# Performance work log

Hardware: AMD Instinct MI355X
Metric: run time of the kernel (lower is better)

## Reference

```python
import jax, jax.numpy as jnp
import numpy as np

N_NODES = 30000
N_EDGES = 300000
C = 16          # multiplicity of input scalars and of each output irrep
SH_SPLITS = [(0, 1), (1, 4), (4, 9)]  # l=0,1,2 slices of edge_sh


def setup_inputs() -> dict:
    key = jax.random.key(0)
    ks = jax.random.split(key, 7)
    node_feat = jax.random.normal(ks[0], (N_NODES, C), dtype=jnp.float32)
    edge_index = jax.random.randint(ks[1], (2, N_EDGES), 0, N_NODES, dtype=jnp.int64)
    edge_sh = jax.random.normal(ks[2], (N_EDGES, 9), dtype=jnp.float32)
    edge_radial = jax.random.uniform(ks[3], (N_EDGES, 16), dtype=jnp.float32)
    W1 = jax.random.normal(ks[4], (16, 64), dtype=jnp.float32)     # radial net layer 1
    W2 = jax.random.normal(ks[5], (64, 3 * C * C), dtype=jnp.float32)  # -> tp.weight_numel = 768
    W_si = jax.random.normal(ks[6], (C, C), dtype=jnp.float32)     # self-interaction 0e->0e
    return {"node_feat": node_feat, "edge_index": edge_index, "edge_sh": edge_sh,
            "edge_radial": edge_radial, "W1": W1, "W2": W2, "W_si": W_si}


def reference(node_feat, edge_index, edge_sh, edge_radial, W1, W2, W_si):
    N, c = node_feat.shape  # c == C
    src, dst = edge_index[0], edge_index[1]

    # Radial MLP (e3nn FullyConnectedNet style: weight / sqrt(fan_in), silu, no bias)
    h = jax.nn.silu(edge_radial @ (W1 / jnp.sqrt(jnp.asarray(W1.shape[0], W1.dtype))))
    tpw = h @ (W2 / jnp.sqrt(jnp.asarray(W2.shape[0], W2.dtype)))  # (E, 768)
    tpw = tpw.reshape(-1, 3, c, c)  # (E, l, u, v)

    # Gather source scalars and mix multiplicities per path (0e x l -> l, CG = identity)
    x = node_feat[src]                                   # (E, C)
    mix = jnp.einsum('eu,eluv->elv', x, tpw) / jnp.sqrt(jnp.asarray(c, x.dtype))  # (E,3,C)

    # Outer product with each SH degree; e3nn mul-major layout (v, m)
    msgs = []
    for l, (a, b) in enumerate(SH_SPLITS):
        m = mix[:, l, :, None] * edge_sh[:, None, a:b]   # (E, C, 2l+1)
        msgs.append(m.reshape(m.shape[0], -1))
    messages = jnp.concatenate(msgs, axis=-1)            # (E, 144)

    # Scatter-add to destination nodes
    agg = jax.ops.segment_sum(messages, dst, num_segments=N)  # (N, 144)

    # Self-interaction: equivariant Linear, only 0e->0e path; l>0 outputs are zero
    si_scalar = node_feat @ (W_si / jnp.sqrt(jnp.asarray(c, node_feat.dtype)))  # (N, C)
    si = jnp.concatenate([si_scalar, jnp.zeros((N, 8 * c), si_scalar.dtype)], axis=-1)
    return agg + si
```

## Files before the change

### kernel.cpp

```cpp
#include <hip/hip_runtime.h>


typedef _Float16 f16x2 __attribute__((ext_vector_type(2)));
typedef _Float16 f16x8 __attribute__((ext_vector_type(8)));
typedef __fp16  g16x2 __attribute__((ext_vector_type(2)));
typedef float f32x4 __attribute__((ext_vector_type(4)));

union AFrag { unsigned int u[4]; f16x2 h2[4]; f16x8 v; };
union BFrag { uint4 u4; f16x8 v; };
union HW { g16x2 g; f16x2 f; unsigned int u; };


__global__ __launch_bounds__(256)
void prep_kernel(const float* __restrict__ W2, const float* __restrict__ W1,
                 _Float16* __restrict__ bfrag, _Float16* __restrict__ w1frag,
                 const int* __restrict__ ei, int* __restrict__ counts, int E) {
    int t = blockIdx.x * 256 + threadIdx.x;
    if (t < E) atomicAdd(&counts[ei[E + t] + 1], 1);
    if (t < 96 * 512) {
        int f = t >> 9;
        int rr = t & 511;
        int lane = rr >> 3, j = rr & 7;
        int ks = f / 3, nt = f - 3 * ks;
        int q = lane >> 4, c = lane & 15;
        int ku = ks * 32 + q * 8 + j;
        int k = ku >> 4, u = ku & 15;
        int n = nt * 16 + c;
        int l = n >> 4, v = n & 15;
        float val = W2[(size_t)k * 768 + l * 256 + u * 16 + v] * 0.03125f;
        bfrag[t] = (_Float16)val;
    }
    if (t < 2048) {
        int nt = t >> 9, rr = t & 511;
        int lane = rr >> 3, j = rr & 7;
        int q = lane >> 4, c = lane & 15;
        int u = q * 8 + j;
        float val = (q < 2) ? W1[u * 64 + nt * 16 + c] * 0.25f : 0.0f;
        w1frag[t] = (_Float16)val;
    }
}

__global__ __launch_bounds__(1024)
void scan_kernel(int* __restrict__ data, int n_pad) {
    __shared__ int wsum[16];
    __shared__ int carry_s;
    int tid = threadIdx.x, lane = tid & 63, wid = tid >> 6;
    if (tid == 0) carry_s = 0;
    __syncthreads();
    for (int base = 0; base < n_pad; base += 32768) {
        int beg = base + tid * 32;
        int4 c0[8];
        #pragma unroll
        for (int j = 0; j < 8; ++j)
            c0[j] = *(const int4*)(data + beg + j * 4);
        int s = 0;
        #pragma unroll
        for (int j = 0; j < 8; ++j) s += c0[j].x + c0[j].y + c0[j].z + c0[j].w;

        int v = s;
        #pragma unroll
        for (int off = 1; off < 64; off <<= 1) {
            int t = __shfl_up(v, off, 64);
            if (lane >= off) v += t;
        }
        if (lane == 63) wsum[wid] = v;
        __syncthreads();
        if (wid == 0 && lane < 16) {
            int w = wsum[lane];
            #pragma unroll
            for (int off = 1; off < 16; off <<= 1) {
                int t = __shfl_up(w, off, 16);
                if (lane >= off) w += t;
            }
            wsum[lane] = w;
        }
        __syncthreads();
        int run = carry_s + (v - s) + (wid > 0 ? wsum[wid - 1] : 0);
        #pragma unroll
        for (int j = 0; j < 8; ++j) {
            int4 o;
            run += c0[j].x; o.x = run;
            run += c0[j].y; o.y = run;
            run += c0[j].z; o.z = run;
            run += c0[j].w; o.w = run;
            *(int4*)(data + beg + j * 4) = o;
        }
        __syncthreads();
        if (tid == 1023) carry_s = run;
        __syncthreads();
    }
}


__global__ __launch_bounds__(64, 4)
void edge_mfma_kernel(const float* __restrict__ nf, const int* __restrict__ ei,
                      const float* __restrict__ radial,
                      const _Float16* __restrict__ w1frag,
                      const float* __restrict__ sh,
                      const _Float16* __restrict__ bfrag,
                      const int* __restrict__ offs, int* __restrict__ curs,
                      _Float16* __restrict__ mixs, _Float16* __restrict__ shs, int E) {
    __shared__ unsigned int h_lds[64][32];

    int lane = threadIdx.x & 63;
    int r_ = lane & 15;
    int q  = lane >> 4;
    int qh = q >> 1;
    int ul = (q & 1) * 8;
    unsigned int sel = qh ? 0x03020302u : 0x01000100u;

    int ebase = blockIdx.x * 64;

    HW xp[4][4];
    #pragma unroll
    for (int m = 0; m < 4; ++m) {
        int e = ebase + m * 16 + r_; if (e >= E) e = E - 1;
        int src = ei[e];
        const float* xpp = nf + (size_t)src * 16 + ul;
        float4 a = *(const float4*)xpp;
        float4 b = *(const float4*)(xpp + 4);
        xp[m][0].g = __builtin_amdgcn_cvt_pkrtz(a.x, a.y);
        xp[m][1].g = __builtin_amdgcn_cvt_pkrtz(a.z, a.w);
        xp[m][2].g = __builtin_amdgcn_cvt_pkrtz(b.x, b.y);
        xp[m][3].g = __builtin_amdgcn_cvt_pkrtz(b.z, b.w);
    }

    int p = 0;
    {
        int e = ebase + lane;
        if (e < E) {
            int dst = ei[E + e];
            p = offs[dst] + atomicAdd(&curs[dst], 1);
            const float* s = sh + (size_t)e * 9;
            float4 s03 = *(const float4*)s;
            float4 s47 = *(const float4*)(s + 4);
            float s8 = s[8];
            unsigned int* d = (unsigned int*)(shs + (size_t)p * 10);
            HW w0, w1, w2, w3, w4;
            w0.g = __builtin_amdgcn_cvt_pkrtz(s03.x, s03.y);
            w1.g = __builtin_amdgcn_cvt_pkrtz(s03.z, s03.w);
            w2.g = __builtin_amdgcn_cvt_pkrtz(s47.x, s47.y);
            w3.g = __builtin_amdgcn_cvt_pkrtz(s47.z, s47.w);
            w4.g = __builtin_amdgcn_cvt_pkrtz(s8, 0.0f);
            d[0] = w0.u; d[1] = w1.u; d[2] = w2.u; d[3] = w3.u; d[4] = w4.u;
        }
    }

    {
        BFrag wf[4];
        #pragma unroll
        for (int nt = 0; nt < 4; ++nt)
            wf[nt].u4 = *(const uint4*)(w1frag + (size_t)nt * 512 + lane * 8);

        #pragma unroll
        for (int m = 0; m < 4; ++m) {
            AFrag ra;
            if (q < 2) {
                int e = ebase + m * 16 + r_; if (e >= E) e = E - 1;
                const float* rp = radial + (size_t)e * 16 + q * 8;
                float4 a = *(const float4*)rp;
                float4 b = *(const float4*)(rp + 4);
                HW t0, t1, t2, t3;
                t0.g = __builtin_amdgcn_cvt_pkrtz(a.x, a.y);
                t1.g = __builtin_amdgcn_cvt_pkrtz(a.z, a.w);
                t2.g = __builtin_amdgcn_cvt_pkrtz(b.x, b.y);
                t3.g = __builtin_amdgcn_cvt_pkrtz(b.z, b.w);
                ra.u[0] = t0.u; ra.u[1] = t1.u; ra.u[2] = t2.u; ra.u[3] = t3.u;
            } else {
                ra.u[0] = 0; ra.u[1] = 0; ra.u[2] = 0; ra.u[3] = 0;
            }
            #pragma unroll
            for (int nt = 0; nt < 4; ++nt) {
                f32x4 z4 = __builtin_amdgcn_mfma_f32_16x16x32_f16(
                    ra.v, wf[nt].v, (f32x4){0.f, 0.f, 0.f, 0.f}, 0, 0, 0);
                #pragma unroll
                for (int i = 0; i < 4; ++i) {
                    float z = z4[i];
                    float h = z * __builtin_amdgcn_rcpf(1.0f + __expf(-z));
                    float hn = __shfl_xor(h, 1);
                    if (!(r_ & 1)) {
                        int el = m * 16 + q * 4 + i;
                        HW w; w.g = __builtin_amdgcn_cvt_pkrtz(h, hn);
                        h_lds[el][((nt << 3) + (r_ >> 1)) ^ (el & 31)] = w.u;
                    }
                }
            }
        }
    }

    f32x4 acc[4][3];
    #pragma unroll
    for (int m = 0; m < 4; ++m)
        #pragma unroll
        for (int nt = 0; nt < 3; ++nt)
            acc[m][nt] = (f32x4){0.f, 0.f, 0.f, 0.f};

    #pragma unroll 2
    for (int ks = 0; ks < 32; ++ks) {
        BFrag b[3];
        #pragma unroll
        for (int nt = 0; nt < 3; ++nt)
            b[nt].u4 = *(const uint4*)(bfrag + (size_t)(ks * 3 + nt) * 512 + lane * 8);
        #pragma unroll
        for (int m = 0; m < 4; ++m) {
            int el = m * 16 + r_;
            unsigned int hw = h_lds[el][ks ^ (el & 31)];
            HW hv; hv.u = __builtin_amdgcn_perm(hw, hw, sel);
            AFrag a;
            #pragma unroll
            for (int p2 = 0; p2 < 4; ++p2)
                a.h2[p2] = hv.f * xp[m][p2].f;
            #pragma unroll
            for (int nt = 0; nt < 3; ++nt)
                acc[m][nt] = __builtin_amdgcn_mfma_f32_16x16x32_f16(a.v, b[nt].v, acc[m][nt], 0, 0, 0);
        }
    }

    unsigned int* mixu = (unsigned int*)mixs;
    #pragma unroll
    for (int m = 0; m < 4; ++m) {
        #pragma unroll
        for (int i = 0; i < 4; ++i) {
            int el = m * 16 + q * 4 + i;
            int e = ebase + el;
            int pe = __shfl(p, el, 64);
            if (e < E) {
                HW pr; pr.g = __builtin_amdgcn_cvt_pkrtz(acc[m][0][i], acc[m][1][i]);
                mixu[(size_t)pe * 24 + r_] = pr.u;
                mixs[(size_t)pe * 48 + 32 + r_] = (_Float16)acc[m][2][i];
            }
        }
    }
}


__global__ __launch_bounds__(256)
void gather_kernel(const _Float16* __restrict__ mixs, const _Float16* __restrict__ shs,
                   const int* __restrict__ offs,
                   const float* __restrict__ nf, const float* __restrict__ Wsi,
                   float* __restrict__ out, int N) {
    int node = blockIdx.x * 4 + (threadIdx.x >> 6);
    if (node >= N) return;
    int lane = threadIdx.x & 63;

    auto chmap = [](int c, int& hi, int& si) {
        if (c < 16)      { hi = 2 * c;           si = 0; }
        else if (c < 64) { int t = c - 16; hi = 2 * (t / 3) + 1; si = 1 + t % 3; }
        else             { int t = c - 64; hi = 32 + t / 5;      si = 4 + t % 5; }
    };
    int hi0, si0, hi1, si1, hi2 = 0, si2 = 0;
    chmap(lane, hi0, si0);
    chmap(lane + 64, hi1, si1);
    if (lane < 16) chmap(lane + 128, hi2, si2);

    float g0[8], g1[8], g2[8];
    #pragma unroll
    for (int j = 0; j < 8; ++j) { g0[j] = 0.f; g1[j] = 0.f; g2[j] = 0.f; }

    int off = offs[node], end = offs[node + 1];
    int i = off;
    for (; i + 7 < end; i += 8) {
        #pragma unroll
        for (int j = 0; j < 8; ++j) {
            const _Float16* m = mixs + (size_t)(i + j) * 48;
            const _Float16* s = shs + (size_t)(i + j) * 10;
            g0[j] = fmaf((float)m[hi0], (float)s[si0], g0[j]);
            g1[j] = fmaf((float)m[hi1], (float)s[si1], g1[j]);
            if (lane < 16) g2[j] = fmaf((float)m[hi2], (float)s[si2], g2[j]);
        }
    }
    for (int j = 0; i < end; ++i, ++j) {
        const _Float16* m = mixs + (size_t)i * 48;
        const _Float16* s = shs + (size_t)i * 10;
        g0[j] = fmaf((float)m[hi0], (float)s[si0], g0[j]);
        g1[j] = fmaf((float)m[hi1], (float)s[si1], g1[j]);
        if (lane < 16) g2[j] = fmaf((float)m[hi2], (float)s[si2], g2[j]);
    }
    float a0 = (g0[0] + g0[1]) + (g0[2] + g0[3]) + ((g0[4] + g0[5]) + (g0[6] + g0[7]));
    float a1 = (g1[0] + g1[1]) + (g1[2] + g1[3]) + ((g1[4] + g1[5]) + (g1[6] + g1[7]));
    float a2 = (g2[0] + g2[1]) + (g2[2] + g2[3]) + ((g2[4] + g2[5]) + (g2[6] + g2[7]));

    if (lane < 16) {
        const float* xr = nf + (size_t)node * 16;
        float si = 0.0f;
        #pragma unroll
        for (int u = 0; u < 16; ++u)
            si = fmaf(xr[u], Wsi[u * 16 + lane], si);
        a0 = fmaf(si, 0.25f, a0);
    }

    float* orow = out + (size_t)node * 144;
    orow[lane] = a0;
    orow[lane + 64] = a1;
    if (lane < 16) orow[lane + 128] = a2;
}


__global__ __launch_bounds__(256)
void si_init_kernel(const float* __restrict__ nf, const float* __restrict__ Wsi,
                    float* __restrict__ out, int N) {
    int t = blockIdx.x * blockDim.x + threadIdx.x;
    int total = N * 144;
    if (t >= total) return;
    int n = t / 144;
    int c = t - n * 144;
    float val = 0.0f;
    if (c < 16) {
        const float* xr = nf + n * 16;
        #pragma unroll
        for (int u = 0; u < 16; ++u)
            val = fmaf(xr[u], Wsi[u * 16 + c], val);
        val *= 0.25f;
    }
    out[t] = val;
}

__global__ __launch_bounds__(256)
void edge_kernel_atomic(const float* __restrict__ nf, const int* __restrict__ ei,
                        const float* __restrict__ sh, const float* __restrict__ radial,
                        const float* __restrict__ W1, const float* __restrict__ W2,
                        float* __restrict__ out, int E) {
    int e = blockIdx.x * blockDim.x + threadIdx.x;
    if (e >= E) return;
    int src = ei[e];
    int dst = ei[E + e];
    float r[16], x[16];
    #pragma unroll
    for (int u = 0; u < 16; ++u) r[u] = radial[e * 16 + u] * 0.25f;
    #pragma unroll
    for (int u = 0; u < 16; ++u) x[u] = nf[src * 16 + u] * 0.03125f;
    float acc[48];
    #pragma unroll
    for (int j = 0; j < 48; ++j) acc[j] = 0.0f;
    for (int k = 0; k < 64; ++k) {
        float z = 0.0f;
        #pragma unroll
        for (int u = 0; u < 16; ++u) z = fmaf(r[u], W1[u * 64 + k], z);
        float hk = z / (1.0f + __expf(-z));
        const float* w2k = W2 + k * 768;
        #pragma unroll 4
        for (int u = 0; u < 16; ++u) {
            float p = hk * x[u];
            const float* w = w2k + u * 16;
            #pragma unroll
            for (int l = 0; l < 3; ++l)
                #pragma unroll
                for (int v = 0; v < 16; ++v)
                    acc[l * 16 + v] = fmaf(p, w[l * 256 + v], acc[l * 16 + v]);
        }
    }
    const float* she = sh + e * 9;
    float* orow = out + (long)dst * 144;
    #pragma unroll
    for (int v = 0; v < 16; ++v) atomicAdd(&orow[v], acc[v] * she[0]);
    #pragma unroll
    for (int v = 0; v < 16; ++v)
        for (int m = 0; m < 3; ++m)
            atomicAdd(&orow[16 + v * 3 + m], acc[16 + v] * she[1 + m]);
    #pragma unroll
    for (int v = 0; v < 16; ++v)
        for (int m = 0; m < 5; ++m)
            atomicAdd(&orow[64 + v * 5 + m], acc[32 + v] * she[4 + m]);
}


extern "C" void kernel_launch(void* const* d_in, const int* in_sizes, int n_in,
                              void* d_out, int out_size, void* d_ws, size_t ws_size,
                              hipStream_t stream) {
    const float* nf     = (const float*)d_in[0];
    const int*   ei     = (const int*)  d_in[1];
    const float* sh     = (const float*)d_in[2];
    const float* radial = (const float*)d_in[3];
    const float* W1     = (const float*)d_in[4];
    const float* W2     = (const float*)d_in[5];
    const float* Wsi    = (const float*)d_in[6];
    float* out = (float*)d_out;

    const int N = in_sizes[0] / 16;
    const int E = in_sizes[1] / 2;

    int n_scan = N + 1;
    int n_pad  = (n_scan + 32767) & ~32767;

    size_t mix_bytes  = (size_t)E * 48 * sizeof(_Float16);
    size_t offs_bytes = (size_t)n_pad * sizeof(int);
    size_t curs_bytes = (size_t)N * sizeof(int);
    size_t shs_bytes  = (size_t)E * 10 * sizeof(_Float16);
    size_t bfrag_off  = (mix_bytes + offs_bytes + curs_bytes + shs_bytes + 127) & ~(size_t)127;
    size_t bfrag_bytes = 96 * 512 * sizeof(_Float16);
    size_t w1f_off    = bfrag_off + bfrag_bytes;
    size_t w1f_bytes  = 2048 * sizeof(_Float16);
    size_t need = w1f_off + w1f_bytes;

    if (ws_size < need) {
        int total = N * 144;
        hipLaunchKernelGGL(si_init_kernel, dim3((total + 255) / 256), dim3(256), 0, stream,
                           nf, Wsi, out, N);
        hipLaunchKernelGGL(edge_kernel_atomic, dim3((E + 255) / 256), dim3(256), 0, stream,
                           nf, ei, sh, radial, W1, W2, out, E);
        return;
    }

    char* wsb = (char*)d_ws;
    _Float16* mixs = (_Float16*)wsb;
    int*   offs = (int*)(wsb + mix_bytes);
    int*   curs = (int*)(wsb + mix_bytes + offs_bytes);
    _Float16* shs = (_Float16*)(wsb + mix_bytes + offs_bytes + curs_bytes);
    _Float16* bfrag = (_Float16*)(wsb + bfrag_off);
    _Float16* w1frag = (_Float16*)(wsb + w1f_off);

    (void)hipMemsetAsync(offs, 0, offs_bytes + curs_bytes, stream);

    int eb256 = (E + 255) / 256;
    hipLaunchKernelGGL(prep_kernel, dim3(eb256), dim3(256), 0, stream,
                       W2, W1, bfrag, w1frag, ei, offs, E);
    hipLaunchKernelGGL(scan_kernel, dim3(1), dim3(1024), 0, stream, offs, n_pad);
    int eb64 = (E + 63) / 64;
    hipLaunchKernelGGL(edge_mfma_kernel, dim3(eb64), dim3(64), 0, stream,
                       nf, ei, radial, w1frag, sh, bfrag, offs, curs, mixs, shs, E);
    hipLaunchKernelGGL(gather_kernel, dim3((N + 3) / 4), dim3(256), 0, stream,
                       mixs, shs, offs, nf, Wsi, out, N);
}
```

Baseline: 132.7 us.

## Accumulate gather messages in packed fp16 with two edges per wavefront

Rewrites the per-node gather so each lane loads packed 32-bit half2 words of mix and SH values, and the wave splits into two 24-lane halves that each process alternate edges. Accumulation runs in packed fp16 and the halves are combined with shuffles at the end. The aim is fewer load instructions and fewer scalar conversions and FMAs per edge. The cost is precision: sums over many edges accumulated in fp16 may lose accuracy or overflow, and the output stores become strided and less coalesced.

```diff
diff --git a/kernel.cpp b/kernel.cpp
--- a/kernel.cpp
+++ b/kernel.cpp
@@ -242,57 +242,95 @@
     int node = blockIdx.x * 4 + (threadIdx.x >> 6);
     if (node >= N) return;
     int lane = threadIdx.x & 63;
-
-    auto chmap = [](int c, int& hi, int& si) {
-        if (c < 16)      { hi = 2 * c;           si = 0; }
-        else if (c < 64) { int t = c - 16; hi = 2 * (t / 3) + 1; si = 1 + t % 3; }
-        else             { int t = c - 64; hi = 32 + t / 5;      si = 4 + t % 5; }
-    };
-    int hi0, si0, hi1, si1, hi2 = 0, si2 = 0;
-    chmap(lane, hi0, si0);
-    chmap(lane + 64, hi1, si1);
-    if (lane < 16) chmap(lane + 128, hi2, si2);
-
-    float g0[8], g1[8], g2[8];
-    #pragma unroll
-    for (int j = 0; j < 8; ++j) { g0[j] = 0.f; g1[j] = 0.f; g2[j] = 0.f; }
+    int half = (lane >= 24 && lane < 48) ? 1 : 0;
+    int w = lane - half * 24;
+    bool active = lane < 48;
+    bool isP = active && (w < 16);
+    bool isQ = active && (w >= 16) && (w < 24);
+    int t = w - 16;
+
+    const unsigned int* mixw = (const unsigned int*)mixs;
+    const unsigned int* shw  = (const unsigned int*)shs;
+
+    HW accP0, accP1; accP0.u = 0; accP1.u = 0;
+    HW accQ0, accQ1, accQ2, accQ3, accQ4, accQ5;
+    accQ0.u = accQ1.u = accQ2.u = accQ3.u = accQ4.u = accQ5.u = 0;
 
     int off = offs[node], end = offs[node + 1];
     int i = off;
+
+    auto do_pair = [&](int ibase, bool pred) {
+        int idx = ibase + half;
+        bool valid = !pred || (idx < end);
+        int ic = valid ? idx : ibase;
+        unsigned int M = 0, Sa = 0, Sb = 0, Sc = 0;
+        if (active) M = mixw[(size_t)ic * 24 + w];
+        if (isP) { Sa = shw[(size_t)ic * 5 + 0]; Sb = shw[(size_t)ic * 5 + 1]; }
+        if (isQ) { Sa = shw[(size_t)ic * 5 + 2]; Sb = shw[(size_t)ic * 5 + 3];
+                   Sc = shw[(size_t)ic * 5 + 4]; }
+        if (!valid) { Sa = 0; Sb = 0; Sc = 0; }
+        HW m_, sa, sb, sc; m_.u = M; sa.u = Sa; sb.u = Sb; sc.u = Sc;
+        if (isP) {
+            accP0.f += m_.f * sa.f;
+            HW mh; mh.u = __builtin_amdgcn_perm(M, M, 0x03020302u);
+            accP1.f += mh.f * sb.f;
+        }
+        if (isQ) {
+            HW ma; ma.u = __builtin_amdgcn_perm(M, M, 0x01000100u);
+            HW mb; mb.u = __builtin_amdgcn_perm(M, M, 0x03020302u);
+            accQ0.f += ma.f * sa.f;
+            accQ1.f += ma.f * sb.f;
+            accQ2.f += ma.f * sc.f;
+            accQ3.f += mb.f * sa.f;
+            accQ4.f += mb.f * sb.f;
+            accQ5.f += mb.f * sc.f;
+        }
+    };
+
     for (; i + 7 < end; i += 8) {
         #pragma unroll
-        for (int j = 0; j < 8; ++j) {
-            const _Float16* m = mixs + (size_t)(i + j) * 48;
-            const _Float16* s = shs + (size_t)(i + j) * 10;
-            g0[j] = fmaf((float)m[hi0], (float)s[si0], g0[j]);
-            g1[j] = fmaf((float)m[hi1], (float)s[si1], g1[j]);
-            if (lane < 16) g2[j] = fmaf((float)m[hi2], (float)s[si2], g2[j]);
-        }
-    }
-    for (int j = 0; i < end; ++i, ++j) {
-        const _Float16* m = mixs + (size_t)i * 48;
-        const _Float16* s = shs + (size_t)i * 10;
-        g0[j] = fmaf((float)m[hi0], (float)s[si0], g0[j]);
-        g1[j] = fmaf((float)m[hi1], (float)s[si1], g1[j]);
-        if (lane < 16) g2[j] = fmaf((float)m[hi2], (float)s[si2], g2[j]);
-    }
-    float a0 = (g0[0] + g0[1]) + (g0[2] + g0[3]) + ((g0[4] + g0[5]) + (g0[6] + g0[7]));
-    float a1 = (g1[0] + g1[1]) + (g1[2] + g1[3]) + ((g1[4] + g1[5]) + (g1[6] + g1[7]));
-    float a2 = (g2[0] + g2[1]) + (g2[2] + g2[3]) + ((g2[4] + g2[5]) + (g2[6] + g2[7]));
-
-    if (lane < 16) {
+        for (int jp = 0; jp < 4; ++jp) do_pair(i + 2 * jp, false);
+    }
+    for (; i < end; i += 2) do_pair(i, true);
+
+    {
+        int o;
+        o = __shfl((int)accP0.u, lane + 24, 64); if (lane < 24) { HW h_; h_.u = (unsigned)o; accP0.f += h_.f; }
+        o = __shfl((int)accP1.u, lane + 24, 64); if (lane < 24) { HW h_; h_.u = (unsigned)o; accP1.f += h_.f; }
+        o = __shfl((int)accQ0.u, lane + 24, 64); if (lane < 24) { HW h_; h_.u = (unsigned)o; accQ0.f += h_.f; }
+        o = __shfl((int)accQ1.u, lane + 24, 64); if (lane < 24) { HW h_; h_.u = (unsigned)o; accQ1.f += h_.f; }
+        o = __shfl((int)accQ2.u, lane + 24, 64); if (lane < 24) { HW h_; h_.u = (unsigned)o; accQ2.f += h_.f; }
+        o = __shfl((int)accQ3.u, lane + 24, 64); if (lane < 24) { HW h_; h_.u = (unsigned)o; accQ3.f += h_.f; }
+        o = __shfl((int)accQ4.u, lane + 24, 64); if (lane < 24) { HW h_; h_.u = (unsigned)o; accQ4.f += h_.f; }
+        o = __shfl((int)accQ5.u, lane + 24, 64); if (lane < 24) { HW h_; h_.u = (unsigned)o; accQ5.f += h_.f; }
+    }
+
+    if (lane >= 24) return;
+    float* orow = out + (size_t)node * 144;
+    if (w < 16) {
+        float c0 = (float)accP0.f[0];
+        float c1 = (float)accP0.f[1];
+        float c2 = (float)accP1.f[0];
+        float c3 = (float)accP1.f[1];
         const float* xr = nf + (size_t)node * 16;
         float si = 0.0f;
         #pragma unroll
         for (int u = 0; u < 16; ++u)
-            si = fmaf(xr[u], Wsi[u * 16 + lane], si);
-        a0 = fmaf(si, 0.25f, a0);
-    }
-
-    float* orow = out + (size_t)node * 144;
-    orow[lane] = a0;
-    orow[lane + 64] = a1;
-    if (lane < 16) orow[lane + 128] = a2;
+            si = fmaf(xr[u], Wsi[u * 16 + w], si);
+        c0 = fmaf(si, 0.25f, c0);
+        orow[w] = c0;
+        orow[16 + 3 * w + 0] = c1;
+        orow[16 + 3 * w + 1] = c2;
+        orow[16 + 3 * w + 2] = c3;
+    } else {
+        float* qp = orow + 64 + 10 * t;
+        qp[0] = (float)accQ0.f[0]; qp[1] = (float)accQ0.f[1];
+        qp[2] = (float)accQ1.f[0]; qp[3] = (float)accQ1.f[1];
+        qp[4] = (float)accQ2.f[0];
+        qp[5] = (float)accQ3.f[0]; qp[6] = (float)accQ3.f[1];
+        qp[7] = (float)accQ4.f[0]; qp[8] = (float)accQ4.f[1];
+        qp[9] = (float)accQ5.f[0];
+    }
 }
 
 
```

Result: faster. 116.8 us (-12.0%).
